# Kernel tuning notes

Hardware: AMD Instinct MI355X
Metric: run time of the kernel (lower is better)

## Reference

```python
import jax, jax.numpy as jnp
import numpy as np

D_MODEL = 2048
N_HEADS = 16
GKV = 4
D_FF = 8192
D_HEAD = D_MODEL // N_HEADS
EPS = 1e-6


def rmsnorm(x, w):
    ms = jnp.mean(x * x, axis=-1, keepdims=True)
    return x * jax.lax.rsqrt(ms + EPS) * w


def attention(q, k, v, mask=None):
    # q: (B,Tq,H,d), k/v: (B,Tk,H,d)
    scale = 1.0 / jnp.sqrt(jnp.asarray(q.shape[-1], q.dtype))
    scores = jnp.einsum('bqhd,bkhd->bhqk', q, k) * scale
    if mask is not None:
        scores = scores + mask
    probs = jax.nn.softmax(scores, axis=-1)
    return jnp.einsum('bhqk,bkhd->bqhd', probs, v)


def setup_inputs() -> dict:
    key = jax.random.key(0)
    ks = jax.random.split(key, 12)
    B, T = 2, 2048
    s = 0.02
    return {
        'x': jax.random.normal(ks[0], (B, T, D_MODEL), jnp.float32),
        'k_ctx': jax.random.normal(ks[1], (B, T, GKV, D_HEAD), jnp.float32),
        'v_ctx': jax.random.normal(ks[2], (B, T, GKV, D_HEAD), jnp.float32),
        # cross-attn params (weights stored as (in, out); y = x @ W)
        'wq': jax.random.normal(ks[3], (D_MODEL, D_MODEL), jnp.float32) * s,
        'wo_cross': jax.random.normal(ks[4], (D_MODEL, D_MODEL), jnp.float32) * s,
        'norm_q_w': jnp.ones((D_MODEL,), jnp.float32),
        # self-attn params
        'wqkv': jax.random.normal(ks[5], (D_MODEL, 3 * D_MODEL), jnp.float32) * s,
        'wo_self': jax.random.normal(ks[6], (D_MODEL, D_MODEL), jnp.float32) * s,
        'norm_qkv_w': jnp.ones((D_MODEL,), jnp.float32),
        # FFN params (bias=False in FeedForward)
        'ffn_w1': jax.random.normal(ks[7], (D_MODEL, D_FF), jnp.float32) * s,
        'ffn_w2': jax.random.normal(ks[8], (D_FF, D_MODEL), jnp.float32) * s,
        'ffn_norm_w': jnp.ones((D_MODEL,), jnp.float32),
    }


def reference(x, k_ctx, v_ctx, wq, wo_cross, norm_q_w, wqkv, wo_self,
              norm_qkv_w, ffn_w1, ffn_w2, ffn_norm_w):
    B, T, D = x.shape
    repeat = N_HEADS // GKV

    # ---- cross attention (GQA) ----
    q = (rmsnorm(x, norm_q_w) @ wq).reshape(B, T, N_HEADS, D_HEAD)
    k = jnp.repeat(k_ctx, repeat, axis=2)  # (B,Tk,H,d), matches repeat_interleave
    v = jnp.repeat(v_ctx, repeat, axis=2)
    ctx = attention(q, k, v, mask=None).reshape(B, T, D)
    x = x + ctx @ wo_cross

    # ---- causal self attention ----
    xn = rmsnorm(x, norm_qkv_w)
    qkv = xn @ wqkv
    qs, ks_, vs = jnp.split(qkv, 3, axis=-1)
    qs = qs.reshape(B, T, N_HEADS, D_HEAD)
    ks_ = ks_.reshape(B, T, N_HEADS, D_HEAD)
    vs = vs.reshape(B, T, N_HEADS, D_HEAD)
    causal_mask = jnp.triu(jnp.full((T, T), -jnp.inf, x.dtype), k=1)[None, None]
    ctx2 = attention(qs, ks_, vs, mask=causal_mask).reshape(B, T, D)
    x = x + ctx2 @ wo_self

    # ---- FFN (SiLU) ----
    h = rmsnorm(x, ffn_norm_w)
    y = jax.nn.silu(h @ ffn_w1) @ ffn_w2
    return x + y
```

## Files before the change

### kernel.cpp

```cpp
#include <hip/hip_runtime.h>
#include <math.h>

typedef unsigned short u16;
typedef __attribute__((ext_vector_type(4))) u16 u16x4;
typedef __attribute__((ext_vector_type(8))) u16 u16x8;
typedef __attribute__((ext_vector_type(8))) __bf16 bf16x8;
typedef __attribute__((ext_vector_type(4))) float f32x4;
typedef __attribute__((ext_vector_type(16))) float f32x16;
typedef __attribute__((ext_vector_type(4))) unsigned u32x4;

#define D_MODEL 2048
#define SEQ 2048
#define BATCH 2
#define NH 16
#define HD 128
#define DFF 8192
#define ROWS (BATCH * SEQ)

__device__ __forceinline__ u16 f2bf(float f) {
  union { float f; unsigned u; } v; v.f = f;
  unsigned r = v.u + 0x7FFFu + ((v.u >> 16) & 1u);
  return (u16)(r >> 16);
}
__device__ __forceinline__ u16 to_bf16(float f) { return f2bf(f); }
__device__ __forceinline__ u16 to_bf16(u16 v) { return v; }

__device__ __forceinline__ f32x4 mfma16(u16x8 a, u16x8 b, f32x4 c) {
  return __builtin_amdgcn_mfma_f32_16x16x32_bf16(
      __builtin_bit_cast(bf16x8, a), __builtin_bit_cast(bf16x8, b), c, 0, 0, 0);
}
__device__ __forceinline__ f32x16 mfma32(u16x8 a, u16x8 b, f32x16 c) {
  return __builtin_amdgcn_mfma_f32_32x32x16_bf16(
      __builtin_bit_cast(bf16x8, a), __builtin_bit_cast(bf16x8, b), c, 0, 0, 0);
}

__device__ __forceinline__ void gll16(const void* g, void* l) {
  __builtin_amdgcn_global_load_lds(
      (const __attribute__((address_space(1))) void*)g,
      (__attribute__((address_space(3))) void*)l, 16, 0, 0);
}

__global__ __launch_bounds__(256) void cast_kernel(const float* __restrict__ in,
                                                   u16* __restrict__ out, int n8) {
  int i = blockIdx.x * 256 + threadIdx.x;
  if (i >= n8) return;
  const float4* p = (const float4*)in + (size_t)i * 2;
  float4 a = p[0], b = p[1];
  u16x8 o;
  o[0] = f2bf(a.x); o[1] = f2bf(a.y); o[2] = f2bf(a.z); o[3] = f2bf(a.w);
  o[4] = f2bf(b.x); o[5] = f2bf(b.y); o[6] = f2bf(b.z); o[7] = f2bf(b.w);
  *((u16x8*)out + i) = o;
}

__global__ __launch_bounds__(256) void cast_transpose_kernel(
    const float* __restrict__ in, u16* __restrict__ out, int K, int N) {
  __shared__ float tile[64][65];
  int n0 = blockIdx.x * 64, k0 = blockIdx.y * 64;
  int tx = threadIdx.x & 63, ty = threadIdx.x >> 6;
#pragma unroll
  for (int i = 0; i < 64; i += 4)
    tile[ty + i][tx] = in[(size_t)(k0 + ty + i) * N + n0 + tx];
  __syncthreads();
#pragma unroll
  for (int i = 0; i < 64; i += 4)
    out[(size_t)(n0 + ty + i) * K + k0 + tx] = f2bf(tile[tx][ty + i]);
}

template <typename ST>
__global__ __launch_bounds__(256) void build_vt_kernel(
    const ST* __restrict__ src, u16* __restrict__ dst, int HZ,
    size_t src_b_stride, size_t src_h_stride, int src_tok_stride) {
  __shared__ u16 tl[64][72];
  int z = blockIdx.z, zb = z / HZ, zh = z % HZ;
  const ST* s = src + (size_t)zb * src_b_stride + (size_t)zh * src_h_stride;
  int t0 = blockIdx.x * 64, d0 = blockIdx.y * 64;
  int rr = threadIdx.x >> 4, cc = (threadIdx.x & 15) * 4;
#pragma unroll
  for (int pp = 0; pp < 4; ++pp) {
    int t = pp * 16 + rr;
    const ST* sp = s + (size_t)(t0 + t) * src_tok_stride + d0 + cc;
#pragma unroll
    for (int j = 0; j < 4; ++j) tl[t][cc + j] = to_bf16(sp[j]);
  }
  __syncthreads();
  u16* dp = dst + (size_t)z * HD * SEQ;
#pragma unroll
  for (int pp = 0; pp < 4; ++pp) {
    int d = pp * 16 + rr;
    u16x4 w;
#pragma unroll
    for (int j = 0; j < 4; ++j) w[j] = tl[cc + j][d];
    *(u16x4*)(dp + (size_t)(d0 + d) * SEQ + t0 + cc) = w;
  }
}

__global__ __launch_bounds__(256) void rmsnorm_kernel(const float* __restrict__ x,
                                                      const float* __restrict__ w,
                                                      u16* __restrict__ out) {
  __shared__ float red[4];
  int row = blockIdx.x, t = threadIdx.x;
  const float4* xr = (const float4*)(x + (size_t)row * D_MODEL);
  float4 a = xr[t * 2], b = xr[t * 2 + 1];
  float ss = a.x * a.x + a.y * a.y + a.z * a.z + a.w * a.w +
             b.x * b.x + b.y * b.y + b.z * b.z + b.w * b.w;
#pragma unroll
  for (int m = 1; m < 64; m <<= 1) ss += __shfl_xor(ss, m, 64);
  if ((t & 63) == 0) red[t >> 6] = ss;
  __syncthreads();
  float tot = red[0] + red[1] + red[2] + red[3];
  float sc = rsqrtf(tot * (1.0f / D_MODEL) + 1e-6f);
  const float4* wr = (const float4*)w;
  float4 wa = wr[t * 2], wb = wr[t * 2 + 1];
  u16x8 o;
  o[0] = f2bf(a.x * sc * wa.x); o[1] = f2bf(a.y * sc * wa.y);
  o[2] = f2bf(a.z * sc * wa.z); o[3] = f2bf(a.w * sc * wa.w);
  o[4] = f2bf(b.x * sc * wb.x); o[5] = f2bf(b.y * sc * wb.y);
  o[6] = f2bf(b.z * sc * wb.z); o[7] = f2bf(b.w * sc * wb.w);
  *((u16x8*)(out + (size_t)row * D_MODEL) + t) = o;
}

#define GPHASE(T, P, VM, ISSUE)                                                \
  {                                                                            \
    if (ISSUE) issue_half(4 * (T) + (P) + 4);                                  \
    asm volatile("s_waitcnt vmcnt(" #VM ")" ::: "memory");                     \
    __builtin_amdgcn_sched_barrier(0);                                         \
    __builtin_amdgcn_s_barrier();                                              \
    if (((P) & 1) == 0) {                                                      \
      const u16* SA = S + (((((T) & 1) << 2) | (((P) >> 1) << 1)) << 13);      \
      const u16* SB = SA + 8192;                                               \
      _Pragma("unroll") for (int m = 0; m < 8; ++m) {                          \
        int row = wm * 128 + m * 16 + r16;                                     \
        aF[m] = *(const u16x8*)(SA + row * 32 + ((kg ^ ((row >> 1) & 3)) << 3)); \
      }                                                                        \
      _Pragma("unroll") for (int n = 0; n < 4; ++n) {                          \
        int row = wn * 64 + n * 16 + r16;                                      \
        bF[n] = *(const u16x8*)(SB + row * 32 + ((kg ^ ((row >> 1) & 3)) << 3)); \
      }                                                                        \
    }                                                                          \
    __builtin_amdgcn_s_setprio(1);                                             \
    _Pragma("unroll") for (int m = 0; m < 8; ++m) {                            \
      acc[m][2 * ((P) & 1)] = mfma16(aF[m], bF[2 * ((P) & 1)], acc[m][2 * ((P) & 1)]); \
      acc[m][2 * ((P) & 1) + 1] =                                              \
          mfma16(aF[m], bF[2 * ((P) & 1) + 1], acc[m][2 * ((P) & 1) + 1]);     \
    }                                                                          \
    __builtin_amdgcn_s_setprio(0);                                             \
    __builtin_amdgcn_s_barrier();                                              \
  }

template <int EPI>
__global__ __launch_bounds__(512, 1) void gemm256_kernel(
    const u16* __restrict__ A, const u16* __restrict__ Bt, void* __restrict__ Cv,
    const float* __restrict__ res, int N, int K) {
  __shared__ __align__(16) u16 S[8 * 8192];
  const int tid = threadIdx.x, lane = tid & 63, wave = tid >> 6;
  const int wm = wave >> 2, wn = wave & 3;
  const int r16 = lane & 15, kg = lane >> 4;
  const int cols = N >> 8;
  const int cpx = gridDim.x >> 3;
  const int bid = blockIdx.x;
  const int swz = (bid & 7) * cpx + (bid >> 3);
  const int bm = (swz / cols) * 256, bn = (swz % cols) * 256;
  const int nt = K >> 6;

  auto issue_half = [&](int h) {
    int p = h & 3, t = h >> 2;
    const u16* src = (p & 1) ? (Bt + (size_t)bn * K) : (A + (size_t)bm * K);
    int kbase = t * 64 + (p >> 1) * 32;
    u16* ldst = S + ((((t & 1) << 2) | p) << 13);
#pragma unroll
    for (int i = 0; i < 2; ++i) {
      int c = i * 512 + tid;
      int row = c >> 2, ch = c & 3;
      int kc = ch ^ ((row >> 1) & 3);
      gll16(src + (size_t)row * K + kbase + kc * 8, ldst + c * 8);
    }
  };

  u16x8 aF[8], bF[4];
  f32x4 acc[8][4] = {};

  issue_half(0); issue_half(1); issue_half(2); issue_half(3);
  for (int t = 0; t < nt - 1; ++t) {
    GPHASE(t, 0, 6, true);
    GPHASE(t, 1, 6, true);
    GPHASE(t, 2, 6, true);
    GPHASE(t, 3, 6, true);
  }
  {
    const int t = nt - 1;
    GPHASE(t, 0, 4, false);
    GPHASE(t, 1, 4, false);
    GPHASE(t, 2, 0, false);
    GPHASE(t, 3, 0, false);
  }

#pragma unroll
  for (int m = 0; m < 8; ++m) {
    int r0 = bm + wm * 128 + m * 16 + kg * 4;
#pragma unroll
    for (int n = 0; n < 4; ++n) {
      int cc = bn + wn * 64 + n * 16 + r16;
#pragma unroll
      for (int r = 0; r < 4; ++r) {
        size_t idx = (size_t)(r0 + r) * N + cc;
        float v = acc[m][n][r];
        if (EPI == 1) {
          ((float*)Cv)[idx] = res[idx] + v;
        } else if (EPI == 0) {
          ((u16*)Cv)[idx] = f2bf(v);
        } else {
          float s = v / (1.0f + __expf(-v));
          ((u16*)Cv)[idx] = f2bf(s);
        }
      }
    }
  }
}

template <bool CAUSAL, bool SELF>
__global__ __launch_bounds__(512, 2) void attn2_kernel(
    const u16* __restrict__ qp, const u16* __restrict__ kp,
    const u16* __restrict__ vtp, u16* __restrict__ outp) {
  __shared__ __align__(16) u16 Kl[64 * 128];
  __shared__ __align__(16) u16 Vl[128 * 64];
  const int tid = threadIdx.x, lane = tid & 63, wave = tid >> 6;
  const int lo = lane & 31, hi = lane >> 5;
  const int qt = blockIdx.x, bh = blockIdx.y, b = bh >> 4, h = bh & 15;
  const int qw0 = qt * 256 + wave * 32;
  const int qg = qw0 + lo;
  const size_t qstr = SELF ? 6144 : 2048;
  const size_t kstr = SELF ? 6144 : 512;
  const u16* qbase = qp + ((size_t)b * SEQ + qg) * qstr + h * HD;
  const u16* kbase = kp + (size_t)b * SEQ * kstr + (SELF ? (2048 + h * HD) : ((h >> 2) * HD));
  const u16* vbase = vtp + (size_t)(SELF ? (b * NH + h) : (b * 4 + (h >> 2))) * HD * SEQ;

  u16x8 qf[8];
#pragma unroll
  for (int dc = 0; dc < 8; ++dc) qf[dc] = *(const u16x8*)(qbase + dc * 16 + hi * 8);

  f32x16 o[4] = {};
  float m_run = -3e38f, l_run = 0.f;
  const int ntiles = CAUSAL ? qt * 4 + 4 : SEQ / 64;
  const float scale = 0.088388347648318447f;

  for (int kt = 0; kt < ntiles; ++kt) {
    __syncthreads();
#pragma unroll
    for (int i = 0; i < 2; ++i) {
      int c = i * 512 + tid;
      int krow = c >> 4, ks = c & 15;
      gll16(kbase + (size_t)(kt * 64 + krow) * kstr + ((ks ^ (krow & 15)) * 8),
            Kl + (size_t)c * 8);
      int vd = c >> 3, vs = c & 7;
      gll16(vbase + (size_t)vd * SEQ + kt * 64 + ((vs ^ (vd & 7)) * 8),
            Vl + (size_t)c * 8);
    }
    __syncthreads();
    if (CAUSAL && kt * 64 > qw0 + 31) continue;

    f32x16 s01[2] = {};
#pragma unroll
    for (int k2 = 0; k2 < 2; ++k2) {
      int key = k2 * 32 + lo;
#pragma unroll
      for (int mf = 0; mf < 8; ++mf) {
        int dc = mf * 2 + hi;
        u16x8 kf = *(const u16x8*)(Kl + key * 128 + ((dc ^ (key & 15)) * 8));
        s01[k2] = mfma32(kf, qf[mf], s01[k2]);
      }
    }

    float sv[32];
    float pm = -3e38f;
#pragma unroll
    for (int k2 = 0; k2 < 2; ++k2)
#pragma unroll
      for (int r = 0; r < 16; ++r) {
        float v = s01[k2][r];
        if (CAUSAL) {
          int key = kt * 64 + k2 * 32 + (r & 3) + 8 * (r >> 2) + 4 * hi;
          if (key > qg) v = -3e38f;
        }
        sv[k2 * 16 + r] = v;
        pm = fmaxf(pm, v);
      }
    pm = fmaxf(pm, __shfl_xor(pm, 32, 64));
    float mn = fmaxf(m_run, pm);
    float corr = __expf((m_run - mn) * scale);
    m_run = mn;

    float ps = 0.f;
    u16x8 pf[4];
#pragma unroll
    for (int k2 = 0; k2 < 2; ++k2)
#pragma unroll
      for (int hf = 0; hf < 2; ++hf) {
        float p8[8];
#pragma unroll
        for (int j = 0; j < 8; ++j) {
          p8[j] = __expf((sv[k2 * 16 + hf * 8 + j] - mn) * scale);
          ps += p8[j];
        }
        unsigned w0, w1, w2, w3;
        asm("v_cvt_pk_bf16_f32 %0, %1, %2" : "=v"(w0) : "v"(p8[0]), "v"(p8[1]));
        asm("v_cvt_pk_bf16_f32 %0, %1, %2" : "=v"(w1) : "v"(p8[2]), "v"(p8[3]));
        asm("v_cvt_pk_bf16_f32 %0, %1, %2" : "=v"(w2) : "v"(p8[4]), "v"(p8[5]));
        asm("v_cvt_pk_bf16_f32 %0, %1, %2" : "=v"(w3) : "v"(p8[6]), "v"(p8[7]));
        asm("v_permlane32_swap_b32 %0, %1" : "+v"(w0), "+v"(w2));
        asm("v_permlane32_swap_b32 %0, %1" : "+v"(w1), "+v"(w3));
        u32x4 fr; fr[0] = w0; fr[1] = w1; fr[2] = w2; fr[3] = w3;
        pf[k2 * 2 + hf] = __builtin_bit_cast(u16x8, fr);
      }
    ps += __shfl_xor(ps, 32, 64);
    l_run = l_run * corr + ps;

#pragma unroll
    for (int mb = 0; mb < 4; ++mb)
#pragma unroll
      for (int r = 0; r < 16; ++r) o[mb][r] *= corr;

#pragma unroll
    for (int kc = 0; kc < 4; ++kc) {
      int vcs = kc * 2 + hi;
#pragma unroll
      for (int mb = 0; mb < 4; ++mb) {
        int d = mb * 32 + lo;
        u16x8 vf = *(const u16x8*)(Vl + d * 64 + ((vcs ^ (d & 7)) * 8));
        o[mb] = mfma32(vf, pf[kc], o[mb]);
      }
    }
  }

  float inv = 1.0f / l_run;
  u16* ob = outp + ((size_t)b * SEQ + qg) * D_MODEL + h * HD + 4 * hi;
#pragma unroll
  for (int mb = 0; mb < 4; ++mb)
#pragma unroll
    for (int rq = 0; rq < 4; ++rq) {
      u16x4 w;
#pragma unroll
      for (int j = 0; j < 4; ++j) w[j] = f2bf(o[mb][rq * 4 + j] * inv);
      *(u16x4*)(ob + mb * 32 + rq * 8) = w;
    }
}

extern "C" void kernel_launch(void* const* d_in, const int* in_sizes, int n_in,
                              void* d_out, int out_size, void* d_ws, size_t ws_size,
                              hipStream_t stream) {
  const float* x          = (const float*)d_in[0];
  const float* k_ctx      = (const float*)d_in[1];
  const float* v_ctx      = (const float*)d_in[2];
  const float* wq         = (const float*)d_in[3];
  const float* wo_cross   = (const float*)d_in[4];
  const float* norm_q_w   = (const float*)d_in[5];
  const float* wqkv       = (const float*)d_in[6];
  const float* wo_self    = (const float*)d_in[7];
  const float* norm_qkv_w = (const float*)d_in[8];
  const float* ffn_w1     = (const float*)d_in[9];
  const float* ffn_w2     = (const float*)d_in[10];
  const float* ffn_norm_w = (const float*)d_in[11];
  float* out = (float*)d_out;

  char* ws = (char*)d_ws;
  size_t off = 0;
  auto alloc_u16 = [&](size_t n) { u16* p = (u16*)(ws + off); off += n * 2; return p; };
  auto alloc_f32 = [&](size_t n) { float* p = (float*)(ws + off); off += n * 4; return p; };
  u16* wq_bf   = alloc_u16((size_t)2048 * 2048);
  u16* woc_bf  = alloc_u16((size_t)2048 * 2048);
  u16* wqkv_bf = alloc_u16((size_t)2048 * 6144);
  u16* wos_bf  = alloc_u16((size_t)2048 * 2048);
  u16* w1_bf   = alloc_u16((size_t)2048 * 8192);
  u16* w2_bf   = alloc_u16((size_t)8192 * 2048);
  u16* xn_bf   = alloc_u16((size_t)ROWS * 2048);
  u16* qkv_bf  = alloc_u16((size_t)ROWS * 6144);
  u16* attn_bf = alloc_u16((size_t)ROWS * 2048);
  float* x1    = alloc_f32((size_t)ROWS * 2048);
  float* x2    = alloc_f32((size_t)ROWS * 2048);
  u16* q_bf    = qkv_bf;
  u16* h1_bf   = qkv_bf;
  u16* kc_bf   = (u16*)x2;
  u16* vt_ctx  = kc_bf + (size_t)BATCH * SEQ * 4 * HD;
  u16* vt_self = xn_bf;

  auto castT = [&](const float* src, u16* dst, int K, int N) {
    cast_transpose_kernel<<<dim3(N / 64, K / 64), 256, 0, stream>>>(src, dst, K, N);
  };
  castT(wq, wq_bf, 2048, 2048);
  castT(wo_cross, woc_bf, 2048, 2048);
  castT(wqkv, wqkv_bf, 2048, 6144);
  castT(wo_self, wos_bf, 2048, 2048);
  castT(ffn_w1, w1_bf, 2048, 8192);
  castT(ffn_w2, w2_bf, 8192, 2048);
  {
    int n8 = (int)((size_t)BATCH * SEQ * 4 * HD / 8);
    cast_kernel<<<dim3((n8 + 255) / 256), dim3(256), 0, stream>>>(k_ctx, kc_bf, n8);
  }
  build_vt_kernel<float><<<dim3(SEQ / 64, HD / 64, BATCH * 4), 256, 0, stream>>>(
      v_ctx, vt_ctx, 4, (size_t)SEQ * 512, (size_t)HD, 512);

  rmsnorm_kernel<<<ROWS, 256, 0, stream>>>(x, norm_q_w, xn_bf);
  gemm256_kernel<0><<<dim3((ROWS / 256) * (2048 / 256)), 512, 0, stream>>>(
      xn_bf, wq_bf, q_bf, nullptr, 2048, 2048);
  attn2_kernel<false, false><<<dim3(SEQ / 256, BATCH * NH), 512, 0, stream>>>(
      q_bf, kc_bf, vt_ctx, attn_bf);
  gemm256_kernel<1><<<dim3((ROWS / 256) * (2048 / 256)), 512, 0, stream>>>(
      attn_bf, woc_bf, x1, x, 2048, 2048);

  rmsnorm_kernel<<<ROWS, 256, 0, stream>>>(x1, norm_qkv_w, xn_bf);
  gemm256_kernel<0><<<dim3((ROWS / 256) * (6144 / 256)), 512, 0, stream>>>(
      xn_bf, wqkv_bf, qkv_bf, nullptr, 6144, 2048);
  build_vt_kernel<u16><<<dim3(SEQ / 64, HD / 64, BATCH * NH), 256, 0, stream>>>(
      qkv_bf + 4096, vt_self, NH, (size_t)SEQ * 6144, (size_t)HD, 6144);
  attn2_kernel<true, true><<<dim3(SEQ / 256, BATCH * NH), 512, 0, stream>>>(
      qkv_bf, qkv_bf, vt_self, attn_bf);
  gemm256_kernel<1><<<dim3((ROWS / 256) * (2048 / 256)), 512, 0, stream>>>(
      attn_bf, wos_bf, x2, x1, 2048, 2048);

  rmsnorm_kernel<<<ROWS, 256, 0, stream>>>(x2, ffn_norm_w, xn_bf);
  gemm256_kernel<2><<<dim3((ROWS / 256) * (8192 / 256)), 512, 0, stream>>>(
      xn_bf, w1_bf, h1_bf, nullptr, 8192, 2048);
  gemm256_kernel<1><<<dim3((ROWS / 256) * (2048 / 256)), 512, 0, stream>>>(
      h1_bf, w2_bf, out, x2, 2048, 8192);
}
```

Measured before the change: 951.1 us.

## Split-K the 2048-wide output GEMMs into two slices plus a combine kernel

The four GEMMs with N=2048 launch only 128 tiles of 256x256, which underfills the GPU's compute units. They now run a split-K of 2, giving 256 blocks that write fp32 partial sums to two scratch buffers. A separate combine kernel then adds the partials, plus the residual or a bf16 cast, to produce the final output. The extra fp32 partial traffic, the added kernel launches and the reuse of scratch buffers by aliasing are the cost of better occupancy.

```diff
diff --git a/kernel.cpp b/kernel.cpp
--- a/kernel.cpp
+++ b/kernel.cpp
@@ -117,6 +117,28 @@
   o[4] = f2bf(b.x * sc * wb.x); o[5] = f2bf(b.y * sc * wb.y);
   o[6] = f2bf(b.z * sc * wb.z); o[7] = f2bf(b.w * sc * wb.w);
   *((u16x8*)(out + (size_t)row * D_MODEL) + t) = o;
+}
+
+template <int MODE>
+__global__ __launch_bounds__(256) void combine_kernel(
+    const float* __restrict__ p0, const float* __restrict__ p1,
+    const float* __restrict__ res, void* __restrict__ outv, int n4) {
+  int i = blockIdx.x * 256 + threadIdx.x;
+  if (i >= n4) return;
+  float4 a = ((const float4*)p0)[i];
+  float4 b = ((const float4*)p1)[i];
+  if (MODE == 1) {
+    float4 r = ((const float4*)res)[i];
+    float4 o;
+    o.x = r.x + a.x + b.x; o.y = r.y + a.y + b.y;
+    o.z = r.z + a.z + b.z; o.w = r.w + a.w + b.w;
+    ((float4*)outv)[i] = o;
+  } else {
+    u16x4 o;
+    o[0] = f2bf(a.x + b.x); o[1] = f2bf(a.y + b.y);
+    o[2] = f2bf(a.z + b.z); o[3] = f2bf(a.w + b.w);
+    ((u16x4*)outv)[i] = o;
+  }
 }
 
 #define GPHASE(T, P, VM, ISSUE)                                                \
@@ -147,10 +169,10 @@
     __builtin_amdgcn_s_barrier();                                              \
   }
 
-template <int EPI>
+template <int EPI, int SPLIT>
 __global__ __launch_bounds__(512, 1) void gemm256_kernel(
     const u16* __restrict__ A, const u16* __restrict__ Bt, void* __restrict__ Cv,
-    const float* __restrict__ res, int N, int K) {
+    float* __restrict__ Cv2, const float* __restrict__ res, int N, int K) {
   __shared__ __align__(16) u16 S[8 * 8192];
   const int tid = threadIdx.x, lane = tid & 63, wave = tid >> 6;
   const int wm = wave >> 2, wn = wave & 3;
@@ -159,13 +181,17 @@
   const int cpx = gridDim.x >> 3;
   const int bid = blockIdx.x;
   const int swz = (bid & 7) * cpx + (bid >> 3);
-  const int bm = (swz / cols) * 256, bn = (swz % cols) * 256;
-  const int nt = K >> 6;
+  const int tiles = gridDim.x / SPLIT;
+  const int tile = swz % tiles, kslice = swz / tiles;
+  const int bm = (tile / cols) * 256, bn = (tile % cols) * 256;
+  const int Ksub = K / SPLIT;
+  const int koff = kslice * Ksub;
+  const int nt = Ksub >> 6;
 
   auto issue_half = [&](int h) {
     int p = h & 3, t = h >> 2;
     const u16* src = (p & 1) ? (Bt + (size_t)bn * K) : (A + (size_t)bm * K);
-    int kbase = t * 64 + (p >> 1) * 32;
+    int kbase = koff + t * 64 + (p >> 1) * 32;
     u16* ldst = S + ((((t & 1) << 2) | p) << 13);
 #pragma unroll
     for (int i = 0; i < 2; ++i) {
@@ -194,6 +220,7 @@
     GPHASE(t, 3, 0, false);
   }
 
+  float* Pp = (EPI == 3) ? (kslice ? Cv2 : (float*)Cv) : nullptr;
 #pragma unroll
   for (int m = 0; m < 8; ++m) {
     int r0 = bm + wm * 128 + m * 16 + kg * 4;
@@ -204,7 +231,9 @@
       for (int r = 0; r < 4; ++r) {
         size_t idx = (size_t)(r0 + r) * N + cc;
         float v = acc[m][n][r];
-        if (EPI == 1) {
+        if (EPI == 3) {
+          Pp[idx] = v;
+        } else if (EPI == 1) {
           ((float*)Cv)[idx] = res[idx] + v;
         } else if (EPI == 0) {
           ((u16*)Cv)[idx] = f2bf(v);
@@ -381,6 +410,9 @@
   u16* kc_bf   = (u16*)x2;
   u16* vt_ctx  = kc_bf + (size_t)BATCH * SEQ * 4 * HD;
   u16* vt_self = xn_bf;
+  float* Pq1  = (float*)((char*)qkv_bf + 16777216);
+  float* Pqkv = (float*)qkv_bf;
+  const int n4 = ROWS * 2048 / 4;
 
   auto castT = [&](const float* src, u16* dst, int K, int N) {
     cast_transpose_kernel<<<dim3(N / 64, K / 64), 256, 0, stream>>>(src, dst, K, N);
@@ -399,26 +431,34 @@
       v_ctx, vt_ctx, 4, (size_t)SEQ * 512, (size_t)HD, 512);
 
   rmsnorm_kernel<<<ROWS, 256, 0, stream>>>(x, norm_q_w, xn_bf);
-  gemm256_kernel<0><<<dim3((ROWS / 256) * (2048 / 256)), 512, 0, stream>>>(
-      xn_bf, wq_bf, q_bf, nullptr, 2048, 2048);
+  gemm256_kernel<3, 2><<<dim3(256), 512, 0, stream>>>(
+      xn_bf, wq_bf, x1, Pq1, nullptr, 2048, 2048);
+  combine_kernel<0><<<dim3((n4 + 255) / 256), 256, 0, stream>>>(
+      x1, Pq1, nullptr, q_bf, n4);
   attn2_kernel<false, false><<<dim3(SEQ / 256, BATCH * NH), 512, 0, stream>>>(
       q_bf, kc_bf, vt_ctx, attn_bf);
-  gemm256_kernel<1><<<dim3((ROWS / 256) * (2048 / 256)), 512, 0, stream>>>(
-      attn_bf, woc_bf, x1, x, 2048, 2048);
+  gemm256_kernel<3, 2><<<dim3(256), 512, 0, stream>>>(
+      attn_bf, woc_bf, x1, Pqkv, nullptr, 2048, 2048);
+  combine_kernel<1><<<dim3((n4 + 255) / 256), 256, 0, stream>>>(
+      x1, Pqkv, x, x1, n4);
 
   rmsnorm_kernel<<<ROWS, 256, 0, stream>>>(x1, norm_qkv_w, xn_bf);
-  gemm256_kernel<0><<<dim3((ROWS / 256) * (6144 / 256)), 512, 0, stream>>>(
-      xn_bf, wqkv_bf, qkv_bf, nullptr, 6144, 2048);
+  gemm256_kernel<0, 1><<<dim3((ROWS / 256) * (6144 / 256)), 512, 0, stream>>>(
+      xn_bf, wqkv_bf, qkv_bf, nullptr, nullptr, 6144, 2048);
   build_vt_kernel<u16><<<dim3(SEQ / 64, HD / 64, BATCH * NH), 256, 0, stream>>>(
       qkv_bf + 4096, vt_self, NH, (size_t)SEQ * 6144, (size_t)HD, 6144);
   attn2_kernel<true, true><<<dim3(SEQ / 256, BATCH * NH), 512, 0, stream>>>(
       qkv_bf, qkv_bf, vt_self, attn_bf);
-  gemm256_kernel<1><<<dim3((ROWS / 256) * (2048 / 256)), 512, 0, stream>>>(
-      attn_bf, wos_bf, x2, x1, 2048, 2048);
+  gemm256_kernel<3, 2><<<dim3(256), 512, 0, stream>>>(
+      attn_bf, wos_bf, x2, Pqkv, nullptr, 2048, 2048);
+  combine_kernel<1><<<dim3((n4 + 255) / 256), 256, 0, stream>>>(
+      x2, Pqkv, x1, x2, n4);
 
   rmsnorm_kernel<<<ROWS, 256, 0, stream>>>(x2, ffn_norm_w, xn_bf);
-  gemm256_kernel<2><<<dim3((ROWS / 256) * (8192 / 256)), 512, 0, stream>>>(
-      xn_bf, w1_bf, h1_bf, nullptr, 8192, 2048);
-  gemm256_kernel<1><<<dim3((ROWS / 256) * (2048 / 256)), 512, 0, stream>>>(
-      h1_bf, w2_bf, out, x2, 2048, 8192);
-}
+  gemm256_kernel<2, 1><<<dim3((ROWS / 256) * (8192 / 256)), 512, 0, stream>>>(
+      xn_bf, w1_bf, h1_bf, nullptr, nullptr, 8192, 2048);
+  gemm256_kernel<3, 2><<<dim3(256), 512, 0, stream>>>(
+      h1_bf, w2_bf, out, x1, nullptr, 2048, 8192);
+  combine_kernel<1><<<dim3((n4 + 255) / 256), 256, 0, stream>>>(
+      out, x1, x2, out, n4);
+}
```

After: 878.4 us. 1.08x faster.
